# Kernel optimization log

Hardware: AMD Instinct MI355X
Metric: run time of the kernel (lower is better)

The kernel has to match this reference:

```python
import jax, jax.numpy as jnp
import numpy as np

B, S, E = 8, 4096, 768
NEG = jnp.float32(-1e30)


def setup_inputs() -> dict:
    key = jax.random.key(0)
    ks = jax.random.split(key, 9)
    full_ebd = jax.random.normal(ks[0], (B, S, E), dtype=jnp.float32)
    # first_idx in [64, S//2): end of question span (question tokens are 1..first_idx-1)
    first = jax.random.randint(ks[1], (B,), 64, S // 2)
    # second_idx in (first, S): end of context span (unused by the math but part of API)
    second = jax.random.randint(ks[2], (B,), S // 2 + 1, S)
    SEQ_idxes = jnp.stack([first, second], axis=1).astype(jnp.int64)
    w = 0.02
    Wq_w = jax.random.normal(ks[3], (E, E), dtype=jnp.float32) * w
    Wq_b = jax.random.normal(ks[4], (E,), dtype=jnp.float32) * w
    Wk_w = jax.random.normal(ks[5], (E, E), dtype=jnp.float32) * w
    Wk_b = jax.random.normal(ks[6], (E,), dtype=jnp.float32) * w
    Wv_w = jax.random.normal(ks[7], (E, E), dtype=jnp.float32) * w
    Wv_b = jax.random.normal(ks[8], (E,), dtype=jnp.float32) * w
    return {"full_ebd": full_ebd, "SEQ_idxes": SEQ_idxes,
            "Wq_w": Wq_w, "Wq_b": Wq_b, "Wk_w": Wk_w, "Wk_b": Wk_b,
            "Wv_w": Wv_w, "Wv_b": Wv_b}


def reference(full_ebd, SEQ_idxes, Wq_w, Wq_b, Wk_w, Wk_b, Wv_w, Wv_b):
    # Vectorized form of the ragged per-sample loop: queries attend to the
    # question tokens 1..first_idx-1 only; masking keys reproduces the slice.
    seq = full_ebd.shape[1]
    inv_sqrt_dk = jnp.float32(1.0 / np.sqrt(full_ebd.shape[-1]))
    Q = full_ebd @ Wq_w.T + Wq_b              # [B,S,E]
    K = full_ebd @ Wk_w.T + Wk_b              # [B,S,E]
    V = full_ebd @ Wv_w.T + Wv_b              # [B,S,E]
    first = SEQ_idxes[:, 0]                   # [B]
    j = jnp.arange(seq)
    key_mask = (j[None, :] >= 1) & (j[None, :] < first[:, None])  # [B,S]
    scores = jnp.einsum('bqe,bke->bqk', Q, K) * inv_sqrt_dk       # [B,S,S]
    scores = jnp.where(key_mask[:, None, :], scores, NEG)
    attn = jax.nn.softmax(scores, axis=-1)
    attn = attn * key_mask[:, None, :].astype(attn.dtype)  # exact zeros outside span
    H = jnp.einsum('bqk,bke->bqe', attn, V)   # [B,S,E]
    return H
```

## Files before the change

kernel.cpp:

```cpp
#include <hip/hip_runtime.h>
#include <hip/hip_bf16.h>
#include <cmath>

typedef __bf16 bf16x8 __attribute__((ext_vector_type(8)));
typedef __bf16 bf16x4 __attribute__((ext_vector_type(4)));
typedef float f32x4 __attribute__((ext_vector_type(4)));

#define GLOBAL_AS __attribute__((address_space(1)))
#define LDS_AS __attribute__((address_space(3)))

__device__ __forceinline__ void async_copy16(const void* g, void* l) {
    __builtin_amdgcn_global_load_lds((const GLOBAL_AS void*)g, (LDS_AS void*)l, 16, 0, 0);
}

__device__ inline int get_first(const int* __restrict__ seq, int b) {
    int stride = (seq[1] == 0) ? 4 : 2;
    return seq[b * stride];
}

__global__ __launch_bounds__(256) void cast_f32_bf16(const float* __restrict__ in,
                                                     __bf16* __restrict__ out, int n4) {
    int i = blockIdx.x * 256 + threadIdx.x;
    if (i >= n4) return;
    float4 v = ((const float4*)in)[i];
    bf16x4 o;
    o[0] = (__bf16)v.x; o[1] = (__bf16)v.y; o[2] = (__bf16)v.z; o[3] = (__bf16)v.w;
    ((bf16x4*)out)[i] = o;
}

__global__ __launch_bounds__(256) void cast3_f32_bf16(
    const float* __restrict__ a, const float* __restrict__ b, const float* __restrict__ c,
    __bf16* __restrict__ oa, __bf16* __restrict__ ob, __bf16* __restrict__ oc, int n4) {
    int i = blockIdx.x * 256 + threadIdx.x;
    if (i >= n4) return;
    const float* in = (blockIdx.y == 0) ? a : (blockIdx.y == 1) ? b : c;
    __bf16* out = (blockIdx.y == 0) ? oa : (blockIdx.y == 1) ? ob : oc;
    float4 v = ((const float4*)in)[i];
    bf16x4 o;
    o[0] = (__bf16)v.x; o[1] = (__bf16)v.y; o[2] = (__bf16)v.z; o[3] = (__bf16)v.w;
    ((bf16x4*)out)[i] = o;
}

__global__ __launch_bounds__(256) void zero_f32(float* __restrict__ p, int n4) {
    int i = blockIdx.x * 256 + threadIdx.x;
    if (i < n4) ((f32x4*)p)[i] = f32x4{0.f, 0.f, 0.f, 0.f};
}

template <int EPI>
__global__ __launch_bounds__(256, 4) void gemm_bt(
    const __bf16* __restrict__ A, int lda, long strideA,
    const __bf16* __restrict__ B, int ldb, long strideB,
    const float* __restrict__ bias,
    void* __restrict__ Cv, int ldc, long strideC,
    int Kfix, const int* __restrict__ seq, int exit_mode, int k_mode,
    float cs, float* __restrict__ rowsum) {
    int z = blockIdx.z;
    int m0 = blockIdx.x * 128, n0 = blockIdx.y * 128;
    int first = seq ? get_first(seq, z) : 0;
    if (exit_mode == 1 && m0 >= first) return;
    if (exit_mode == 2 && n0 >= first) return;
    int K = k_mode ? ((first + 63) & ~63) : Kfix;

    __shared__ char As[16384];
    __shared__ char Bs[16384];

    int tid = threadIdx.x;
    int lane = tid & 63, wid = tid >> 6;
    int waveM = (wid & 1) << 6, waveN = (wid >> 1) << 6;
    int quad = lane >> 4, l16 = lane & 15;

    int r0 = tid >> 3;
    int c8 = (tid & 7) ^ (r0 & 7);
    const __bf16* Ag = A + (long)z * strideA + (long)(m0 + r0) * lda + c8 * 8;
    const __bf16* Bg = B + (long)z * strideB + (long)(n0 + r0) * ldb + c8 * 8;

    f32x4 acc[4][4] = {};
    int xorv = (l16 & 7) << 4;

    for (int k0 = 0; k0 < K; k0 += 64) {
        __syncthreads();
#pragma unroll
        for (int r = 0; r < 4; ++r) {
            async_copy16(Ag + (long)(r * 32) * lda + k0, As + (tid + r * 256) * 16);
            async_copy16(Bg + (long)(r * 32) * ldb + k0, Bs + (tid + r * 256) * 16);
        }
        __syncthreads();
#pragma unroll
        for (int s = 0; s < 2; ++s) {
            int chunk = (((s << 2) + quad) << 4) ^ xorv;
            bf16x8 bfr[4];
#pragma unroll
            for (int j = 0; j < 4; ++j)
                bfr[j] = *(const bf16x8*)(Bs + (waveN + j * 16 + l16) * 128 + chunk);
#pragma unroll
            for (int i = 0; i < 4; ++i) {
                bf16x8 af = *(const bf16x8*)(As + (waveM + i * 16 + l16) * 128 + chunk);
#pragma unroll
                for (int j = 0; j < 4; ++j)
                    acc[i][j] = __builtin_amdgcn_mfma_f32_16x16x32_bf16(af, bfr[j], acc[i][j], 0, 0, 0);
            }
        }
    }

    if (EPI == 0) {
        __bf16* C = (__bf16*)Cv + (long)z * strideC;
#pragma unroll
        for (int i = 0; i < 4; ++i) {
            int rowb = m0 + waveM + i * 16 + quad * 4;
#pragma unroll
            for (int j = 0; j < 4; ++j) {
                int col = n0 + waveN + j * 16 + l16;
                float bv_ = bias[col];
#pragma unroll
                for (int r = 0; r < 4; ++r)
                    C[(long)(rowb + r) * ldc + col] = (__bf16)(acc[i][j][r] + bv_);
            }
        }
    } else if (EPI == 1) {
        __bf16* C = (__bf16*)Cv + (long)z * strideC;
#pragma unroll
        for (int i = 0; i < 4; ++i) {
            int rowb = m0 + waveM + i * 16 + quad * 4;
#pragma unroll
            for (int j = 0; j < 4; ++j) {
                int col = n0 + waveN + j * 16 + l16;
                float bv_ = bias[col];
                bf16x4 o;
#pragma unroll
                for (int r = 0; r < 4; ++r) o[r] = (__bf16)(acc[i][j][r] + bv_);
                *(bf16x4*)&C[(long)col * ldc + rowb] = o;
            }
        }
    } else if (EPI == 2) {
        __bf16* C = (__bf16*)Cv + (long)z * strideC;
        float* rs = rowsum + (long)z * 4096;
#pragma unroll
        for (int i = 0; i < 4; ++i) {
            int rowb = m0 + waveM + i * 16 + quad * 4;
            float sum[4] = {0.f, 0.f, 0.f, 0.f};
#pragma unroll
            for (int j = 0; j < 4; ++j) {
                int col = n0 + waveN + j * 16 + l16;
                bool valid = (col >= 1) && (col < first);
#pragma unroll
                for (int r = 0; r < 4; ++r) {
                    float e = valid ? exp2f(acc[i][j][r] * cs) : 0.0f;
                    __bf16 pb = (__bf16)e;
                    C[(long)(rowb + r) * ldc + col] = pb;
                    sum[r] += (float)pb;
                }
            }
#pragma unroll
            for (int r = 0; r < 4; ++r) {
                float v = sum[r];
                v += __shfl_xor(v, 8); v += __shfl_xor(v, 4);
                v += __shfl_xor(v, 2); v += __shfl_xor(v, 1);
                if (l16 == 0) atomicAdd(&rs[rowb + r], v);
            }
        }
    } else {
        float* C = (float*)Cv + (long)z * strideC;
        const float* rs = rowsum + (long)z * 4096;
#pragma unroll
        for (int i = 0; i < 4; ++i) {
            int rowb = m0 + waveM + i * 16 + quad * 4;
            float inv[4];
#pragma unroll
            for (int r = 0; r < 4; ++r) inv[r] = 1.0f / rs[rowb + r];
#pragma unroll
            for (int j = 0; j < 4; ++j) {
                int col = n0 + waveN + j * 16 + l16;
#pragma unroll
                for (int r = 0; r < 4; ++r)
                    C[(long)(rowb + r) * ldc + col] = acc[i][j][r] * inv[r];
            }
        }
    }
}

extern "C" void kernel_launch(void* const* d_in, const int* in_sizes, int n_in,
                              void* d_out, int out_size, void* d_ws, size_t ws_size,
                              hipStream_t stream) {
    const int B = 8, S = 4096, E = 768, SK = 2048;
    const float* ebd  = (const float*)d_in[0];
    const int*   seq  = (const int*)d_in[1];
    const float* Wq_w = (const float*)d_in[2];
    const float* Wq_b = (const float*)d_in[3];
    const float* Wk_w = (const float*)d_in[4];
    const float* Wk_b = (const float*)d_in[5];
    const float* Wv_w = (const float*)d_in[6];
    const float* Wv_b = (const float*)d_in[7];
    float* out = (float*)d_out;

    char* p = (char*)d_ws;
    __bf16* ebd_bf = (__bf16*)p; p += (size_t)B * S * E * 2;
    __bf16* wq = (__bf16*)p;     p += (size_t)E * E * 2;
    __bf16* wk = (__bf16*)p;     p += (size_t)E * E * 2;
    __bf16* wv = (__bf16*)p;     p += (size_t)E * E * 2;
    __bf16* Qb = (__bf16*)p;     p += (size_t)B * S * E * 2;
    __bf16* Kb = (__bf16*)p;     p += (size_t)B * SK * E * 2;
    __bf16* VT = (__bf16*)p;     p += (size_t)B * E * SK * 2;
    __bf16* Pb = (__bf16*)p;     p += (size_t)B * S * SK * 2;
    float* rowsum = (float*)p;   p += (size_t)B * S * 4;

    zero_f32<<<B * S / 4 / 256, 256, 0, stream>>>(rowsum, B * S / 4);
    cast_f32_bf16<<<(B * S * E / 4 + 255) / 256, 256, 0, stream>>>(ebd, ebd_bf, B * S * E / 4);
    cast3_f32_bf16<<<dim3((E * E / 4 + 255) / 256, 3), 256, 0, stream>>>(
        Wq_w, Wk_w, Wv_w, wq, wk, wv, E * E / 4);

    float cs = (1.0f / sqrtf((float)E)) * 1.44269504088896f;

    gemm_bt<0><<<dim3(B * S / 128, E / 128, 1), 256, 0, stream>>>(
        ebd_bf, E, 0, wq, E, 0, Wq_b, Qb, E, 0, E, nullptr, 0, 0, 0.f, nullptr);
    gemm_bt<0><<<dim3(SK / 128, E / 128, B), 256, 0, stream>>>(
        ebd_bf, E, (long)S * E, wk, E, 0, Wk_b, Kb, E, (long)SK * E, E, seq, 1, 0, 0.f, nullptr);
    gemm_bt<1><<<dim3(SK / 128, E / 128, B), 256, 0, stream>>>(
        ebd_bf, E, (long)S * E, wv, E, 0, Wv_b, VT, SK, (long)E * SK, E, seq, 1, 0, 0.f, nullptr);
    gemm_bt<2><<<dim3(S / 128, SK / 128, B), 256, 0, stream>>>(
        Qb, E, (long)S * E, Kb, E, (long)SK * E, nullptr, Pb, SK, (long)S * SK, E, seq, 2, 0, cs, rowsum);
    gemm_bt<3><<<dim3(S / 128, E / 128, B), 256, 0, stream>>>(
        Pb, SK, (long)S * SK, VT, SK, (long)E * SK, nullptr, out, E, (long)S * E, 0, seq, 0, 1, 0.f, rowsum);
}
```

Measured before the change: 410.3 us.

## Merge prep kernels, fuse K/V projections, add XCD swizzle and fast exp2

Folds the three cast and zero kernels into one prep launch, and merges the K and V projection GEMMs into a single launch using a doubled z-grid. Adds an XCD-aware block remapping for the score and PV GEMMs so neighbouring tiles share L2 on the same die. Also switches the softmax exponent to the hardware exp2 intrinsic and uses pointer increments in the K loop. The aim is to cut launch overhead and improve cache locality; the cost is more branching inside kernels, and the swizzle assumes the block count divides evenly by 8.

```diff
diff --git a/kernel.cpp b/kernel.cpp
--- a/kernel.cpp
+++ b/kernel.cpp
@@ -18,32 +18,47 @@
     return seq[b * stride];
 }
 
-__global__ __launch_bounds__(256) void cast_f32_bf16(const float* __restrict__ in,
-                                                     __bf16* __restrict__ out, int n4) {
-    int i = blockIdx.x * 256 + threadIdx.x;
-    if (i >= n4) return;
-    float4 v = ((const float4*)in)[i];
-    bf16x4 o;
-    o[0] = (__bf16)v.x; o[1] = (__bf16)v.y; o[2] = (__bf16)v.z; o[3] = (__bf16)v.w;
-    ((bf16x4*)out)[i] = o;
-}
-
-__global__ __launch_bounds__(256) void cast3_f32_bf16(
-    const float* __restrict__ a, const float* __restrict__ b, const float* __restrict__ c,
-    __bf16* __restrict__ oa, __bf16* __restrict__ ob, __bf16* __restrict__ oc, int n4) {
-    int i = blockIdx.x * 256 + threadIdx.x;
-    if (i >= n4) return;
-    const float* in = (blockIdx.y == 0) ? a : (blockIdx.y == 1) ? b : c;
-    __bf16* out = (blockIdx.y == 0) ? oa : (blockIdx.y == 1) ? ob : oc;
-    float4 v = ((const float4*)in)[i];
-    bf16x4 o;
-    o[0] = (__bf16)v.x; o[1] = (__bf16)v.y; o[2] = (__bf16)v.z; o[3] = (__bf16)v.w;
-    ((bf16x4*)out)[i] = o;
-}
-
-__global__ __launch_bounds__(256) void zero_f32(float* __restrict__ p, int n4) {
-    int i = blockIdx.x * 256 + threadIdx.x;
-    if (i < n4) ((f32x4*)p)[i] = f32x4{0.f, 0.f, 0.f, 0.f};
+__device__ inline void xcd_swizzle(int& bx, int& by, int& bz) {
+    int gx = gridDim.x, gy = gridDim.y;
+    int nwg = gx * gy * (int)gridDim.z;
+    int flat = bx + gx * (by + gy * bz);
+    int q = nwg >> 3;
+    flat = (flat & 7) * q + (flat >> 3);
+    bx = flat % gx;
+    int t = flat / gx;
+    by = t % gy;
+    bz = t / gy;
+}
+
+#define NB_E 24576
+#define NB_W 576
+#define NB_Z 32
+__global__ __launch_bounds__(256) void prep(
+    const float* __restrict__ ebd, __bf16* __restrict__ ebd_bf,
+    const float* __restrict__ wq_f, const float* __restrict__ wk_f,
+    const float* __restrict__ wv_f,
+    __bf16* __restrict__ wq, __bf16* __restrict__ wk, __bf16* __restrict__ wv,
+    float* __restrict__ rowsum) {
+    int bid = blockIdx.x;
+    if (bid < NB_E) {
+        int i = bid * 256 + threadIdx.x;
+        float4 v = ((const float4*)ebd)[i];
+        bf16x4 o;
+        o[0] = (__bf16)v.x; o[1] = (__bf16)v.y; o[2] = (__bf16)v.z; o[3] = (__bf16)v.w;
+        ((bf16x4*)ebd_bf)[i] = o;
+    } else if (bid < NB_E + 3 * NB_W) {
+        int w = (bid - NB_E) / NB_W;
+        int i = ((bid - NB_E) % NB_W) * 256 + threadIdx.x;
+        const float* in = (w == 0) ? wq_f : (w == 1) ? wk_f : wv_f;
+        __bf16* out = (w == 0) ? wq : (w == 1) ? wk : wv;
+        float4 v = ((const float4*)in)[i];
+        bf16x4 o;
+        o[0] = (__bf16)v.x; o[1] = (__bf16)v.y; o[2] = (__bf16)v.z; o[3] = (__bf16)v.w;
+        ((bf16x4*)out)[i] = o;
+    } else {
+        int i = (bid - NB_E - 3 * NB_W) * 256 + threadIdx.x;
+        ((f32x4*)rowsum)[i] = f32x4{0.f, 0.f, 0.f, 0.f};
+    }
 }
 
 template <int EPI>
@@ -53,9 +68,11 @@
     const float* __restrict__ bias,
     void* __restrict__ Cv, int ldc, long strideC,
     int Kfix, const int* __restrict__ seq, int exit_mode, int k_mode,
-    float cs, float* __restrict__ rowsum) {
-    int z = blockIdx.z;
-    int m0 = blockIdx.x * 128, n0 = blockIdx.y * 128;
+    float cs, float* __restrict__ rowsum, int swz) {
+    int bx = blockIdx.x, by = blockIdx.y, bz = blockIdx.z;
+    if (swz) xcd_swizzle(bx, by, bz);
+    int z = bz;
+    int m0 = bx * 128, n0 = by * 128;
     int first = seq ? get_first(seq, z) : 0;
     if (exit_mode == 1 && m0 >= first) return;
     if (exit_mode == 2 && n0 >= first) return;
@@ -81,9 +98,10 @@
         __syncthreads();
 #pragma unroll
         for (int r = 0; r < 4; ++r) {
-            async_copy16(Ag + (long)(r * 32) * lda + k0, As + (tid + r * 256) * 16);
-            async_copy16(Bg + (long)(r * 32) * ldb + k0, Bs + (tid + r * 256) * 16);
-        }
+            async_copy16(Ag + (long)(r * 32) * lda, As + (tid + r * 256) * 16);
+            async_copy16(Bg + (long)(r * 32) * ldb, Bs + (tid + r * 256) * 16);
+        }
+        Ag += 64; Bg += 64;
         __syncthreads();
 #pragma unroll
         for (int s = 0; s < 2; ++s) {
@@ -144,7 +162,7 @@
                 bool valid = (col >= 1) && (col < first);
 #pragma unroll
                 for (int r = 0; r < 4; ++r) {
-                    float e = valid ? exp2f(acc[i][j][r] * cs) : 0.0f;
+                    float e = valid ? __builtin_amdgcn_exp2f(acc[i][j][r] * cs) : 0.0f;
                     __bf16 pb = (__bf16)e;
                     C[(long)(rowb + r) * ldc + col] = pb;
                     sum[r] += (float)pb;
@@ -173,6 +191,97 @@
 #pragma unroll
                 for (int r = 0; r < 4; ++r)
                     C[(long)(rowb + r) * ldc + col] = acc[i][j][r] * inv[r];
+            }
+        }
+    }
+}
+
+__global__ __launch_bounds__(256, 4) void gemm_kv(
+    const __bf16* __restrict__ A, int lda, long strideA,
+    const __bf16* __restrict__ Bk, const __bf16* __restrict__ Bv,
+    const float* __restrict__ bk, const float* __restrict__ bv,
+    __bf16* __restrict__ Ck, __bf16* __restrict__ CvT,
+    int Kfix, const int* __restrict__ seq) {
+    const int SK = 2048, E = 768;
+    int zz = blockIdx.z;
+    int isv = (zz >= 8);
+    int z = zz & 7;
+    int m0 = blockIdx.x * 128, n0 = blockIdx.y * 128;
+    int first = get_first(seq, z);
+    if (m0 >= first) return;
+
+    __shared__ char As[16384];
+    __shared__ char Bs[16384];
+
+    int tid = threadIdx.x;
+    int lane = tid & 63, wid = tid >> 6;
+    int waveM = (wid & 1) << 6, waveN = (wid >> 1) << 6;
+    int quad = lane >> 4, l16 = lane & 15;
+
+    int r0 = tid >> 3;
+    int c8 = (tid & 7) ^ (r0 & 7);
+    const __bf16* Ag = A + (long)z * strideA + (long)(m0 + r0) * lda + c8 * 8;
+    const __bf16* Bm = isv ? Bv : Bk;
+    const __bf16* Bg = Bm + (long)(n0 + r0) * lda + c8 * 8;
+
+    f32x4 acc[4][4] = {};
+    int xorv = (l16 & 7) << 4;
+
+    for (int k0 = 0; k0 < Kfix; k0 += 64) {
+        __syncthreads();
+#pragma unroll
+        for (int r = 0; r < 4; ++r) {
+            async_copy16(Ag + (long)(r * 32) * lda, As + (tid + r * 256) * 16);
+            async_copy16(Bg + (long)(r * 32) * lda, Bs + (tid + r * 256) * 16);
+        }
+        Ag += 64; Bg += 64;
+        __syncthreads();
+#pragma unroll
+        for (int s = 0; s < 2; ++s) {
+            int chunk = (((s << 2) + quad) << 4) ^ xorv;
+            bf16x8 bfr[4];
+#pragma unroll
+            for (int j = 0; j < 4; ++j)
+                bfr[j] = *(const bf16x8*)(Bs + (waveN + j * 16 + l16) * 128 + chunk);
+#pragma unroll
+            for (int i = 0; i < 4; ++i) {
+                bf16x8 af = *(const bf16x8*)(As + (waveM + i * 16 + l16) * 128 + chunk);
+#pragma unroll
+                for (int j = 0; j < 4; ++j)
+                    acc[i][j] = __builtin_amdgcn_mfma_f32_16x16x32_bf16(af, bfr[j], acc[i][j], 0, 0, 0);
+            }
+        }
+    }
+
+    if (!isv) {
+        __bf16* C = Ck + (long)z * SK * E;
+        const float* bias = bk;
+#pragma unroll
+        for (int i = 0; i < 4; ++i) {
+            int rowb = m0 + waveM + i * 16 + quad * 4;
+#pragma unroll
+            for (int j = 0; j < 4; ++j) {
+                int col = n0 + waveN + j * 16 + l16;
+                float bv_ = bias[col];
+#pragma unroll
+                for (int r = 0; r < 4; ++r)
+                    C[(long)(rowb + r) * E + col] = (__bf16)(acc[i][j][r] + bv_);
+            }
+        }
+    } else {
+        __bf16* C = CvT + (long)z * E * SK;
+        const float* bias = bv;
+#pragma unroll
+        for (int i = 0; i < 4; ++i) {
+            int rowb = m0 + waveM + i * 16 + quad * 4;
+#pragma unroll
+            for (int j = 0; j < 4; ++j) {
+                int col = n0 + waveN + j * 16 + l16;
+                float bv_ = bias[col];
+                bf16x4 o;
+#pragma unroll
+                for (int r = 0; r < 4; ++r) o[r] = (__bf16)(acc[i][j][r] + bv_);
+                *(bf16x4*)&C[(long)col * SK + rowb] = o;
             }
         }
     }
@@ -203,21 +312,17 @@
     __bf16* Pb = (__bf16*)p;     p += (size_t)B * S * SK * 2;
     float* rowsum = (float*)p;   p += (size_t)B * S * 4;
 
-    zero_f32<<<B * S / 4 / 256, 256, 0, stream>>>(rowsum, B * S / 4);
-    cast_f32_bf16<<<(B * S * E / 4 + 255) / 256, 256, 0, stream>>>(ebd, ebd_bf, B * S * E / 4);
-    cast3_f32_bf16<<<dim3((E * E / 4 + 255) / 256, 3), 256, 0, stream>>>(
-        Wq_w, Wk_w, Wv_w, wq, wk, wv, E * E / 4);
+    prep<<<NB_E + 3 * NB_W + NB_Z, 256, 0, stream>>>(
+        ebd, ebd_bf, Wq_w, Wk_w, Wv_w, wq, wk, wv, rowsum);
 
     float cs = (1.0f / sqrtf((float)E)) * 1.44269504088896f;
 
     gemm_bt<0><<<dim3(B * S / 128, E / 128, 1), 256, 0, stream>>>(
-        ebd_bf, E, 0, wq, E, 0, Wq_b, Qb, E, 0, E, nullptr, 0, 0, 0.f, nullptr);
-    gemm_bt<0><<<dim3(SK / 128, E / 128, B), 256, 0, stream>>>(
-        ebd_bf, E, (long)S * E, wk, E, 0, Wk_b, Kb, E, (long)SK * E, E, seq, 1, 0, 0.f, nullptr);
-    gemm_bt<1><<<dim3(SK / 128, E / 128, B), 256, 0, stream>>>(
-        ebd_bf, E, (long)S * E, wv, E, 0, Wv_b, VT, SK, (long)E * SK, E, seq, 1, 0, 0.f, nullptr);
+        ebd_bf, E, 0, wq, E, 0, Wq_b, Qb, E, 0, E, nullptr, 0, 0, 0.f, nullptr, 0);
+    gemm_kv<<<dim3(SK / 128, E / 128, 2 * B), 256, 0, stream>>>(
+        ebd_bf, E, (long)S * E, wk, wv, Wk_b, Wv_b, Kb, VT, E, seq);
     gemm_bt<2><<<dim3(S / 128, SK / 128, B), 256, 0, stream>>>(
-        Qb, E, (long)S * E, Kb, E, (long)SK * E, nullptr, Pb, SK, (long)S * SK, E, seq, 2, 0, cs, rowsum);
+        Qb, E, (long)S * E, Kb, E, (long)SK * E, nullptr, Pb, SK, (long)S * SK, E, seq, 2, 0, cs, rowsum, 1);
     gemm_bt<3><<<dim3(S / 128, E / 128, B), 256, 0, stream>>>(
-        Pb, SK, (long)S * SK, VT, SK, (long)E * SK, nullptr, out, E, (long)S * E, 0, seq, 0, 1, 0.f, rowsum);
-}
+        Pb, SK, (long)S * SK, VT, SK, (long)E * SK, nullptr, out, E, (long)S * E, 0, seq, 0, 1, 0.f, rowsum, 1);
+}
```

After: 480.3 us. 17.0% more time.
